# Optimization experiments

Hardware: AMD Instinct MI355X
Metric: run time of the kernel (lower is better)

## Reference

```python
import jax, jax.numpy as jnp
import numpy as np

HEADS = 12
DIM = 64
NEG = 1e12


def _rope(x, sin, cos):
    # x: [B,T,H,d]; sin/cos: [T,d] (interleaved, each freq repeated twice)
    x2 = jnp.stack([-x[..., 1::2], x[..., ::2]], axis=-1).reshape(x.shape)
    return x * cos[None, :, None, :] + x2 * sin[None, :, None, :]


def setup_inputs() -> dict:
    key = jax.random.key(0)
    k1, k2 = jax.random.split(key, 2)
    hidden_states = jax.random.normal(k1, (8, 1024, 768), dtype=jnp.float32)
    attention_mask = jnp.ones((8, 1024), dtype=jnp.int32)
    W = jax.random.normal(k2, (768, HEADS * DIM * 2), dtype=jnp.float32) * 0.02
    b = jnp.zeros((HEADS * DIM * 2,), dtype=jnp.float32)
    return {"hidden_states": hidden_states, "attention_mask": attention_mask, "W": W, "b": b}


def reference(hidden_states, attention_mask, W, b):
    B, T, D = hidden_states.shape
    H, d = HEADS, DIM
    proj = hidden_states @ W + b                      # [B,T,2*H*d]
    proj = proj.reshape(B, T, H, 2 * d)
    qw, kw = proj[..., :d], proj[..., d:]             # [B,T,H,d] each

    # sinusoidal interleaved RoPE tables
    pos = jnp.arange(T, dtype=jnp.float32)[:, None]                     # [T,1]
    inv_freq = jnp.power(10000.0, -2.0 * jnp.arange(d // 2, dtype=jnp.float32) / d)
    ang = pos * inv_freq                                                # [T,d/2]
    sin = jnp.repeat(jnp.sin(ang), 2, axis=-1)                          # [T,d]
    cos = jnp.repeat(jnp.cos(ang), 2, axis=-1)                          # [T,d]

    qw = _rope(qw, sin, cos)
    kw = _rope(kw, sin, cos)

    logits = jnp.einsum('bmhd,bnhd->bhmn', qw, kw)    # [B,H,T,T]

    # pad mask along key axis (matches torch expand of [B,1,1,T])
    m = attention_mask.astype(logits.dtype)[:, None, None, :]
    logits = logits * m - (1.0 - m) * NEG

    # strict lower-triangular mask (spans with start > end)
    tri = jnp.tril(jnp.ones((T, T), dtype=logits.dtype), -1)
    logits = logits - tri * NEG

    return logits / (d ** 0.5)
```

## Files before the change

### kernel.cpp

```cpp
#include <hip/hip_runtime.h>

#define NEG 1000000000000.0f

typedef __attribute__((ext_vector_type(4))) float f32x4;
typedef __attribute__((ext_vector_type(8))) short bf16x8;

__device__ __forceinline__ unsigned short f2bf(float f) {
    union { float f; unsigned u; } a;
    a.f = f;
    unsigned u = a.u;
    return (unsigned short)((u + 0x7FFFu + ((u >> 16) & 1u)) >> 16);
}

__device__ __forceinline__ void gload_lds16(const void* g, void* l) {
    __builtin_amdgcn_global_load_lds(
        (const __attribute__((address_space(1))) unsigned int*)g,
        (__attribute__((address_space(3))) unsigned int*)l, 16, 0, 0);
}

__global__ void cvt_bf16_kernel(const float* __restrict__ in,
                                unsigned short* __restrict__ out, int n4) {
    int i = blockIdx.x * blockDim.x + threadIdx.x;
    if (i < n4) {
        float4 v = ((const float4*)in)[i];
        ushort4 o;
        o.x = f2bf(v.x); o.y = f2bf(v.y); o.z = f2bf(v.z); o.w = f2bf(v.w);
        ((ushort4*)out)[i] = o;
    }
}

__global__ void transpose_w_kernel(const float* __restrict__ W,
                                   unsigned short* __restrict__ Wt) {
    __shared__ float tile[32][33];
    int n0 = blockIdx.x * 32, k0 = blockIdx.y * 32;
    int tx = threadIdx.x & 31, ty = threadIdx.x >> 5;
    #pragma unroll
    for (int r = 0; r < 32; r += 8)
        tile[ty + r][tx] = W[(k0 + ty + r) * 1536 + n0 + tx];
    __syncthreads();
    #pragma unroll
    for (int r = 0; r < 32; r += 8)
        Wt[(n0 + ty + r) * 768 + k0 + tx] = f2bf(tile[tx][ty + r]);
}

__global__ void rope_table_kernel(float* __restrict__ cosT, float* __restrict__ sinT) {
    int idx = blockIdx.x * blockDim.x + threadIdx.x;
    int t = idx >> 5, i = idx & 31;
    float inv = powf(10000.0f, -(float)i / 32.0f);
    float ang = (float)t * inv;
    cosT[idx] = cosf(ang);
    sinT[idx] = sinf(ang);
}

__global__ __launch_bounds__(256) void proj_rope_kernel(
    const unsigned short* __restrict__ A,
    const unsigned short* __restrict__ Bt,
    const float* __restrict__ bias,
    const float* __restrict__ cosT, const float* __restrict__ sinT,
    unsigned short* __restrict__ qout, unsigned short* __restrict__ kout)
{
    __shared__ unsigned short As[128 * 64];
    __shared__ unsigned short Bs[128 * 64];
    const int tid = threadIdx.x;
    const int lane = tid & 63, w = tid >> 6;
    const int wm = w >> 1, wn = w & 1;
    const int bm = blockIdx.y * 128, bn = blockIdx.x * 128;
    const int l15 = lane & 15, l4 = lane >> 4;

    int crow[4], gcol[4], lbase[4];
    #pragma unroll
    for (int i = 0; i < 4; ++i) {
        int c = i * 256 + w * 64 + lane;
        crow[i] = c >> 3;
        gcol[i] = ((c & 7) ^ (crow[i] & 7)) * 8;
        lbase[i] = (i * 256 + w * 64) * 8;
    }

    f32x4 acc[4][4] = {};
    const int swr = l15 & 7;

    for (int k0 = 0; k0 < 768; k0 += 64) {
        __syncthreads();
        #pragma unroll
        for (int i = 0; i < 4; ++i) {
            gload_lds16(&A[(size_t)(bm + crow[i]) * 768 + k0 + gcol[i]], &As[lbase[i]]);
            gload_lds16(&Bt[(size_t)(bn + crow[i]) * 768 + k0 + gcol[i]], &Bs[lbase[i]]);
        }
        __syncthreads();
        #pragma unroll
        for (int ks = 0; ks < 2; ++ks) {
            bf16x8 af[4], bq[4];
            #pragma unroll
            for (int i = 0; i < 4; ++i) {
                const int ar = wm * 64 + i * 16 + l15;
                const int br = wn * 64 + i * 16 + l15;
                const int cc = (ks * 4 + l4) ^ swr;
                af[i] = *(const bf16x8*)&As[(ar * 8 + cc) * 8];
                bq[i] = *(const bf16x8*)&Bs[(br * 8 + cc) * 8];
            }
            #pragma unroll
            for (int i = 0; i < 4; ++i)
                #pragma unroll
                for (int j = 0; j < 4; ++j)
                    acc[i][j] = __builtin_amdgcn_mfma_f32_16x16x32_bf16(
                        af[i], bq[j], acc[i][j], 0, 0, 0);
        }
    }

    const int rbase = bm + wm * 64 + l4 * 4;
    const int cbase = bn + wn * 64 + l15;
    #pragma unroll
    for (int mi = 0; mi < 4; ++mi) {
        #pragma unroll
        for (int ni = 0; ni < 4; ++ni) {
            const int n = cbase + ni * 16;
            const float bv = bias[n];
            const int h = n >> 7, ww = n & 127;
            const int d = ww & 63, fi = d >> 1;
            unsigned short* __restrict__ dst = (ww < 64) ? qout : kout;
            #pragma unroll
            for (int j = 0; j < 4; ++j) {
                const int m = rbase + mi * 16 + j;
                const int t = m & 1023, bb = m >> 10;
                float v = acc[mi][ni][j] + bv;
                float p = __shfl_xor(v, 1, 64);
                float c = cosT[t * 32 + fi], s = sinT[t * 32 + fi];
                float r = (d & 1) ? fmaf(v, c, p * s) : fmaf(v, c, -p * s);
                dst[((bb * 12 + h) * 1024 + t) * 64 + d] = f2bf(r);
            }
        }
    }
}

__global__ __launch_bounds__(256) void logits_kernel(
    const unsigned short* __restrict__ q, const unsigned short* __restrict__ k,
    const int* __restrict__ mask, float* __restrict__ out)
{
    __shared__ unsigned short Qs[128 * 64];
    __shared__ unsigned short Ks[128 * 64];
    const int tid = threadIdx.x;
    const int lane = tid & 63, w = tid >> 6;
    const int wm = w >> 1, wn = w & 1;
    const int tn = blockIdx.x, tm = blockIdx.y, z = blockIdx.z;
    const int bb = z / 12;
    const int l15 = lane & 15, l4 = lane >> 4;

    #pragma unroll
    for (int i = 0; i < 4; ++i) {
        int c = i * 256 + w * 64 + lane;
        int r = c >> 3;
        int gcol = ((c & 7) ^ (r & 7)) * 8;
        int lb = (i * 256 + w * 64) * 8;
        gload_lds16(&q[(size_t)(z * 1024 + tm * 128 + r) * 64 + gcol], &Qs[lb]);
        gload_lds16(&k[(size_t)(z * 1024 + tn * 128 + r) * 64 + gcol], &Ks[lb]);
    }
    __syncthreads();

    f32x4 acc[4][4] = {};
    const int swr = l15 & 7;
    #pragma unroll
    for (int ks = 0; ks < 2; ++ks) {
        bf16x8 af[4], bq[4];
        #pragma unroll
        for (int i = 0; i < 4; ++i) {
            const int ar = wm * 64 + i * 16 + l15;
            const int br = wn * 64 + i * 16 + l15;
            const int cc = (ks * 4 + l4) ^ swr;
            af[i] = *(const bf16x8*)&Qs[(ar * 8 + cc) * 8];
            bq[i] = *(const bf16x8*)&Ks[(br * 8 + cc) * 8];
        }
        #pragma unroll
        for (int i = 0; i < 4; ++i)
            #pragma unroll
            for (int j = 0; j < 4; ++j)
                acc[i][j] = __builtin_amdgcn_mfma_f32_16x16x32_bf16(
                    af[i], bq[j], acc[i][j], 0, 0, 0);
    }

    const int rbase = tm * 128 + wm * 64 + l4 * 4;
    const int cbase = tn * 128 + wn * 64 + l15;
    float* __restrict__ po = out + (size_t)(z * 1024 + rbase) * 1024 + cbase;
    #pragma unroll
    for (int ni = 0; ni < 4; ++ni) {
        const int n = cbase + ni * 16;
        const float mv = (float)mask[bb * 1024 + n];
        const float addc = -(1.0f - mv) * NEG;
        #pragma unroll
        for (int mi = 0; mi < 4; ++mi) {
            #pragma unroll
            for (int j = 0; j < 4; ++j) {
                const int m = rbase + mi * 16 + j;
                float s = acc[mi][ni][j];
                po[(size_t)(mi * 16 + j) * 1024 + ni * 16] =
                    (s * mv + addc - (n < m ? NEG : 0.0f)) * 0.125f;
            }
        }
    }
}

extern "C" void kernel_launch(void* const* d_in, const int* in_sizes, int n_in,
                              void* d_out, int out_size, void* d_ws, size_t ws_size,
                              hipStream_t stream) {
    const float* hs   = (const float*)d_in[0];
    const int*   mask = (const int*)d_in[1];
    const float* W    = (const float*)d_in[2];
    const float* bias = (const float*)d_in[3];
    float* out = (float*)d_out;

    char* ws = (char*)d_ws;
    unsigned short* qbuf = (unsigned short*)(ws + 0);
    unsigned short* kbuf = (unsigned short*)(ws + 12582912);
    unsigned short* hsb  = (unsigned short*)(ws + 25165824);
    unsigned short* wtb  = (unsigned short*)(ws + 37748736);
    float* cosT = (float*)(ws + 40108032);
    float* sinT = (float*)(ws + 40239104);

    cvt_bf16_kernel<<<6291456 / 4 / 256, 256, 0, stream>>>(hs, hsb, 6291456 / 4);
    transpose_w_kernel<<<dim3(48, 24), 256, 0, stream>>>(W, wtb);
    rope_table_kernel<<<128, 256, 0, stream>>>(cosT, sinT);
    proj_rope_kernel<<<dim3(12, 64), 256, 0, stream>>>(hsb, wtb, bias, cosT, sinT,
                                                       qbuf, kbuf);
    logits_kernel<<<dim3(8, 8, 96), 256, 0, stream>>>(qbuf, kbuf, mask, out);
}
```

Before: 523.6 us.

## Skip matmul for fully-masked lower tiles and load Q/K fragments directly

Tiles lying strictly below the diagonal (tn < tm) now skip the Q·K^T product and write constant mask values with float4 stores. Because every element in such a tile has n < m, the causal term dominates and the result depends only on the pad mask, so the matmul there is unnecessary. The remaining tiles drop the LDS staging and barrier and read bf16x8 MFMA fragments straight from global memory. This avoids about half of the MFMA work and the shared-memory round trip. The risk is uncoalesced global fragment loads, since the skipped tiles still have to write their full output.

```diff
diff --git a/kernel.cpp b/kernel.cpp
--- a/kernel.cpp
+++ b/kernel.cpp
@@ -136,38 +136,43 @@
     const unsigned short* __restrict__ q, const unsigned short* __restrict__ k,
     const int* __restrict__ mask, float* __restrict__ out)
 {
-    __shared__ unsigned short Qs[128 * 64];
-    __shared__ unsigned short Ks[128 * 64];
     const int tid = threadIdx.x;
+    const int tn = blockIdx.x, tm = blockIdx.y, z = blockIdx.z;
+    const int bb = z / 12;
+
+    if (tn < tm) {
+        const int c4 = (tid & 31) * 4;
+        const int r0 = tid >> 5;
+        const int nb = tn * 128 + c4;
+        float4 v;
+        #pragma unroll
+        for (int e = 0; e < 4; ++e) {
+            float mv = (float)mask[bb * 1024 + nb + e];
+            float addc = -(1.0f - mv) * NEG;
+            ((float*)&v)[e] = (addc - NEG) * 0.125f;
+        }
+        float* __restrict__ base = out + (size_t)(z * 1024 + tm * 128) * 1024 + nb;
+        #pragma unroll
+        for (int r = 0; r < 16; ++r)
+            *(float4*)&base[(size_t)(r * 8 + r0) * 1024] = v;
+        return;
+    }
+
     const int lane = tid & 63, w = tid >> 6;
     const int wm = w >> 1, wn = w & 1;
-    const int tn = blockIdx.x, tm = blockIdx.y, z = blockIdx.z;
-    const int bb = z / 12;
     const int l15 = lane & 15, l4 = lane >> 4;
 
-    #pragma unroll
-    for (int i = 0; i < 4; ++i) {
-        int c = i * 256 + w * 64 + lane;
-        int r = c >> 3;
-        int gcol = ((c & 7) ^ (r & 7)) * 8;
-        int lb = (i * 256 + w * 64) * 8;
-        gload_lds16(&q[(size_t)(z * 1024 + tm * 128 + r) * 64 + gcol], &Qs[lb]);
-        gload_lds16(&k[(size_t)(z * 1024 + tn * 128 + r) * 64 + gcol], &Ks[lb]);
-    }
-    __syncthreads();
-
     f32x4 acc[4][4] = {};
-    const int swr = l15 & 7;
+    const unsigned short* __restrict__ qb = q + (size_t)(z * 1024 + tm * 128) * 64;
+    const unsigned short* __restrict__ kb = k + (size_t)(z * 1024 + tn * 128) * 64;
+
     #pragma unroll
     for (int ks = 0; ks < 2; ++ks) {
         bf16x8 af[4], bq[4];
         #pragma unroll
         for (int i = 0; i < 4; ++i) {
-            const int ar = wm * 64 + i * 16 + l15;
-            const int br = wn * 64 + i * 16 + l15;
-            const int cc = (ks * 4 + l4) ^ swr;
-            af[i] = *(const bf16x8*)&Qs[(ar * 8 + cc) * 8];
-            bq[i] = *(const bf16x8*)&Ks[(br * 8 + cc) * 8];
+            af[i] = *(const bf16x8*)&qb[(size_t)(wm * 64 + i * 16 + l15) * 64 + ks * 32 + l4 * 8];
+            bq[i] = *(const bf16x8*)&kb[(size_t)(wn * 64 + i * 16 + l15) * 64 + ks * 32 + l4 * 8];
         }
         #pragma unroll
         for (int i = 0; i < 4; ++i)
```

Result: no change. 527.5 us (+0.7%).
